# Optimization experiments

Measured on AMD Instinct MI355X. Metric: run time of the kernel, lower is better.

The kernel has to match this reference:

```python
import jax, jax.numpy as jnp
import numpy as np

N, K, D = 16384, 32, 256
NEG_SLOPE = 0.01  # torch F.leaky_relu default


def setup_inputs() -> dict:
    key = jax.random.key(0)
    k1, k2, k3, k4 = jax.random.split(key, 4)
    scale = 1.0 / np.sqrt(D)
    return {
        "target": jax.random.normal(k1, (N, D), dtype=jnp.float32),
        "middle": jax.random.normal(k2, (N, K, D), dtype=jnp.float32),
        "W": jax.random.normal(k3, (D, D), dtype=jnp.float32) * scale,
        "b": jnp.zeros((D,), dtype=jnp.float32),
        "a_w": jax.random.normal(k4, (1, D), dtype=jnp.float32) * scale,
        "a_b": jnp.zeros((1,), dtype=jnp.float32),
    }


def reference(target, middle, W, b, a_w, a_b):
    # attention_weight applied to both target and middle (bias added to each,
    # matching the torch code which sums two Linear outputs)
    pt = target @ W.T + b              # [N, D]
    pm = middle @ W.T + b              # [N, K, D]
    h = pt[:, None, :] + pm            # [N, K, D]
    # a_weight: D -> 1
    score = h @ a_w.T + a_b            # [N, K, 1]
    score = jax.nn.leaky_relu(score, negative_slope=NEG_SLOPE)
    coef = jax.nn.softmax(score, axis=-2)   # softmax over neighbor dim K
    neighbor_feature = jnp.sum(coef * middle, axis=-2)  # [N, D]
    return neighbor_feature
```

## Files before the change

kernel.cpp:

```cpp
#include <hip/hip_runtime.h>

#define N_ 16384
#define K_ 32
#define D_ 256
#define NEG_SLOPE 0.01f

__global__ __launch_bounds__(1024) void prep_kernel(
    const float* __restrict__ W, const float* __restrict__ b,
    const float* __restrict__ a_w, const float* __restrict__ a_b,
    float* __restrict__ ws) {
  __shared__ float part[4][D_];
  const int t = threadIdx.x;
  const int dd = t >> 8;
  const int e = t & 255;
  float acc = 0.f;
#pragma unroll 8
  for (int j = 0; j < 64; ++j) {
    const int d = dd * 64 + j;
    acc += a_w[d] * W[d * D_ + e];
  }
  part[dd][e] = acc;
  __syncthreads();
  if (t < D_) ws[t] = part[0][t] + part[1][t] + part[2][t] + part[3][t];
  __syncthreads();
  if (t < D_) part[0][t] = b[t] * a_w[t];
  __syncthreads();
  if (t == 0) {
    float s = 0.f;
    for (int i = 0; i < D_; ++i) s += part[0][i];
    ws[D_] = 2.f * s + a_b[0];
  }
}

__global__ __launch_bounds__(256) void attn_agg_kernel(
    const float* __restrict__ target, const float* __restrict__ middle,
    const float* __restrict__ ws, float* __restrict__ out) {
  __shared__ __align__(16) float smid[K_ * D_];
  __shared__ __align__(16) float lv[D_];
  __shared__ float sdot[K_];
  __shared__ float stp[4];
  __shared__ float scoef[K_];

  const int n = blockIdx.x;
  const int t = threadIdx.x;
  const int r = t >> 3;
  const int c = t & 7;

  lv[t] = ws[t];
  __syncthreads();

  const float4* mrow = (const float4*)(middle + (size_t)n * K_ * D_);
  float pdot = 0.f;
#pragma unroll
  for (int i = 0; i < 8; ++i) {
    const int s = c + i * 8;
    const float4 m4 = mrow[r * 64 + s];
    const float4 v4 = *(const float4*)(lv + s * 4);
    pdot += m4.x * v4.x + m4.y * v4.y + m4.z * v4.z + m4.w * v4.w;
    const int p = s ^ (r & 7);
    *(float4*)(smid + r * D_ + p * 4) = m4;
  }
  pdot += __shfl_xor(pdot, 1);
  pdot += __shfl_xor(pdot, 2);
  pdot += __shfl_xor(pdot, 4);
  if (c == 0) sdot[r] = pdot;

  float tp = target[(size_t)n * D_ + t] * lv[t];
#pragma unroll
  for (int off = 1; off < 64; off <<= 1) tp += __shfl_xor(tp, off);
  if ((t & 63) == 0) stp[t >> 6] = tp;
  __syncthreads();

  if (t < 64) {
    const float tdot = stp[0] + stp[1] + stp[2] + stp[3];
    const float cadd = ws[D_];
    const int k = t & 31;
    float sc = sdot[k] + tdot + cadd;
    sc = sc > 0.f ? sc : NEG_SLOPE * sc;
    float mx = sc;
    mx = fmaxf(mx, __shfl_xor(mx, 1));
    mx = fmaxf(mx, __shfl_xor(mx, 2));
    mx = fmaxf(mx, __shfl_xor(mx, 4));
    mx = fmaxf(mx, __shfl_xor(mx, 8));
    mx = fmaxf(mx, __shfl_xor(mx, 16));
    float ex = __expf(sc - mx);
    float sum = ex;
    sum += __shfl_xor(sum, 1);
    sum += __shfl_xor(sum, 2);
    sum += __shfl_xor(sum, 4);
    sum += __shfl_xor(sum, 8);
    sum += __shfl_xor(sum, 16);
    if (t < 32) scoef[k] = ex / sum;
  }
  __syncthreads();

  float acc = 0.f;
  const int s2 = t >> 2;
  const int e2 = t & 3;
#pragma unroll
  for (int k = 0; k < K_; ++k) {
    const int p = s2 ^ (k & 7);
    acc += scoef[k] * smid[k * D_ + p * 4 + e2];
  }
  out[(size_t)n * D_ + t] = acc;
}

extern "C" void kernel_launch(void* const* d_in, const int* in_sizes, int n_in,
                              void* d_out, int out_size, void* d_ws, size_t ws_size,
                              hipStream_t stream) {
  const float* target = (const float*)d_in[0];
  const float* middle = (const float*)d_in[1];
  const float* W      = (const float*)d_in[2];
  const float* b      = (const float*)d_in[3];
  const float* a_w    = (const float*)d_in[4];
  const float* a_b    = (const float*)d_in[5];
  float* out = (float*)d_out;
  float* ws  = (float*)d_ws;

  prep_kernel<<<1, 1024, 0, stream>>>(W, b, a_w, a_b, ws);
  attn_agg_kernel<<<N_, 256, 0, stream>>>(target, middle, ws, out);
}
```

Measured before the change: 111.1 us.

## Process eight rows per block with register double-buffered prefetch of next row

Each block now handles eight consecutive rows instead of one, with the grid reduced accordingly. While one row is processed through shared memory, the next row's middle and target data are already being loaded into registers (A/B ping-pong), overlapping global loads with compute. This aims to hide memory latency and amortize the per-block setup of loading the folded weight vector. The cost is higher register use (two 8-float4 buffers per thread), which may reduce occupancy, plus an extra barrier per row.

```diff
diff --git a/kernel.cpp b/kernel.cpp
--- a/kernel.cpp
+++ b/kernel.cpp
@@ -4,6 +4,9 @@
 #define K_ 32
 #define D_ 256
 #define NEG_SLOPE 0.01f
+
+#define GRID_ 2048
+#define ITER_ 8
 
 __global__ __launch_bounds__(1024) void prep_kernel(
     const float* __restrict__ W, const float* __restrict__ b,
@@ -32,40 +35,39 @@
   }
 }
 
-__global__ __launch_bounds__(256) void attn_agg_kernel(
-    const float* __restrict__ target, const float* __restrict__ middle,
-    const float* __restrict__ ws, float* __restrict__ out) {
-  __shared__ __align__(16) float smid[K_ * D_];
-  __shared__ __align__(16) float lv[D_];
-  __shared__ float sdot[K_];
-  __shared__ float stp[4];
-  __shared__ float scoef[K_];
+struct Buf {
+  float4 m[8];
+  float tg;
+};
 
-  const int n = blockIdx.x;
-  const int t = threadIdx.x;
-  const int r = t >> 3;
-  const int c = t & 7;
+__device__ __forceinline__ void load_buf(
+    Buf& bf, const float* __restrict__ middle, const float* __restrict__ target,
+    int n, int t, int r, int c) {
+  const float4* mrow = (const float4*)(middle + (size_t)n * K_ * D_);
+#pragma unroll
+  for (int i = 0; i < 8; ++i) bf.m[i] = mrow[r * 64 + c + i * 8];
+  bf.tg = target[(size_t)n * D_ + t];
+}
 
-  lv[t] = ws[t];
-  __syncthreads();
-
-  const float4* mrow = (const float4*)(middle + (size_t)n * K_ * D_);
+__device__ __forceinline__ void process(
+    const Buf& bf, float* __restrict__ smid, const float* __restrict__ lv,
+    float* __restrict__ sdot, float* __restrict__ stp, float* __restrict__ scoef,
+    float cadd, float* __restrict__ outrow, int t, int r, int c) {
   float pdot = 0.f;
 #pragma unroll
   for (int i = 0; i < 8; ++i) {
     const int s = c + i * 8;
-    const float4 m4 = mrow[r * 64 + s];
+    const float4 m4 = bf.m[i];
+    *(float4*)(smid + r * D_ + ((s ^ (r & 7)) * 4)) = m4;
     const float4 v4 = *(const float4*)(lv + s * 4);
     pdot += m4.x * v4.x + m4.y * v4.y + m4.z * v4.z + m4.w * v4.w;
-    const int p = s ^ (r & 7);
-    *(float4*)(smid + r * D_ + p * 4) = m4;
   }
   pdot += __shfl_xor(pdot, 1);
   pdot += __shfl_xor(pdot, 2);
   pdot += __shfl_xor(pdot, 4);
   if (c == 0) sdot[r] = pdot;
 
-  float tp = target[(size_t)n * D_ + t] * lv[t];
+  float tp = bf.tg * lv[t];
 #pragma unroll
   for (int off = 1; off < 64; off <<= 1) tp += __shfl_xor(tp, off);
   if ((t & 63) == 0) stp[t >> 6] = tp;
@@ -73,7 +75,6 @@
 
   if (t < 64) {
     const float tdot = stp[0] + stp[1] + stp[2] + stp[3];
-    const float cadd = ws[D_];
     const int k = t & 31;
     float sc = sdot[k] + tdot + cadd;
     sc = sc > 0.f ? sc : NEG_SLOPE * sc;
@@ -99,10 +100,44 @@
   const int e2 = t & 3;
 #pragma unroll
   for (int k = 0; k < K_; ++k) {
-    const int p = s2 ^ (k & 7);
-    acc += scoef[k] * smid[k * D_ + p * 4 + e2];
+    acc += scoef[k] * smid[k * D_ + ((s2 ^ (k & 7)) * 4) + e2];
   }
-  out[(size_t)n * D_ + t] = acc;
+  outrow[t] = acc;
+  __syncthreads();
+}
+
+__global__ __launch_bounds__(256) void attn_agg_kernel(
+    const float* __restrict__ target, const float* __restrict__ middle,
+    const float* __restrict__ ws, float* __restrict__ out) {
+  __shared__ __align__(16) float smid[K_ * D_];
+  __shared__ __align__(16) float lv[D_];
+  __shared__ float sdot[K_];
+  __shared__ float stp[4];
+  __shared__ float scoef[K_];
+
+  const int t = threadIdx.x;
+  const int r = t >> 3;
+  const int c = t & 7;
+
+  lv[t] = ws[t];
+  const float cadd = ws[D_];
+  __syncthreads();
+
+  const int n0 = blockIdx.x * ITER_;
+
+  Buf A, B;
+  load_buf(A, middle, target, n0, t, r, c);
+
+#pragma unroll 1
+  for (int it = 0; it < ITER_; it += 2) {
+    load_buf(B, middle, target, n0 + it + 1, t, r, c);
+    process(A, smid, lv, sdot, stp, scoef, cadd,
+            out + (size_t)(n0 + it) * D_, t, r, c);
+    if (it + 2 < ITER_)
+      load_buf(A, middle, target, n0 + it + 2, t, r, c);
+    process(B, smid, lv, sdot, stp, scoef, cadd,
+            out + (size_t)(n0 + it + 1) * D_, t, r, c);
+  }
 }
 
 extern "C" void kernel_launch(void* const* d_in, const int* in_sizes, int n_in,
@@ -118,5 +153,5 @@
   float* ws  = (float*)d_ws;
 
   prep_kernel<<<1, 1024, 0, stream>>>(W, b, a_w, a_b, ws);
-  attn_agg_kernel<<<N_, 256, 0, stream>>>(target, middle, ws, out);
+  attn_agg_kernel<<<GRID_, 256, 0, stream>>>(target, middle, ws, out);
 }
```

After: 123.5 us. 11.2% more time.

## Keep middle rows in registers instead of staging through shared memory

Applied to the files above, without the earlier changes.

Each warp now loads 8 neighbor rows of middle as float4 values into registers and computes the score dots with a transposed shuffle-reduction tree. The weighted sum is then done from registers, and the four partial sums per warp are combined through a small shared array. This removes the 32 KB shared-memory staging buffer and its swizzled reads and writes, which should raise occupancy and cut LDS traffic. The cost is higher register pressure from 32 live floats per thread, plus an extra barrier for the final reduction.

```diff
diff --git a/kernel.cpp b/kernel.cpp
--- a/kernel.cpp
+++ b/kernel.cpp
@@ -35,45 +35,62 @@
 __global__ __launch_bounds__(256) void attn_agg_kernel(
     const float* __restrict__ target, const float* __restrict__ middle,
     const float* __restrict__ ws, float* __restrict__ out) {
-  __shared__ __align__(16) float smid[K_ * D_];
-  __shared__ __align__(16) float lv[D_];
+  __shared__ __align__(16) float part[4][D_];
   __shared__ float sdot[K_];
+  __shared__ float scoef[K_];
   __shared__ float stp[4];
-  __shared__ float scoef[K_];
 
+  const int t = threadIdx.x;
+  const int kg = t >> 6;
+  const int l = t & 63;
   const int n = blockIdx.x;
-  const int t = threadIdx.x;
-  const int r = t >> 3;
-  const int c = t & 7;
 
-  lv[t] = ws[t];
-  __syncthreads();
+  const float4* m4p = (const float4*)(middle + (size_t)n * K_ * D_);
+  float4 m[8];
+#pragma unroll
+  for (int j = 0; j < 8; ++j) m[j] = m4p[(kg * 8 + j) * 64 + l];
 
-  const float4* mrow = (const float4*)(middle + (size_t)n * K_ * D_);
-  float pdot = 0.f;
+  const float4 vv = ((const float4*)ws)[l];
+  const float vt = ws[t];
+  const float cadd = ws[D_];
+  const float tg = target[(size_t)n * D_ + t];
+
+  float pd[8];
 #pragma unroll
-  for (int i = 0; i < 8; ++i) {
-    const int s = c + i * 8;
-    const float4 m4 = mrow[r * 64 + s];
-    const float4 v4 = *(const float4*)(lv + s * 4);
-    pdot += m4.x * v4.x + m4.y * v4.y + m4.z * v4.z + m4.w * v4.w;
-    const int p = s ^ (r & 7);
-    *(float4*)(smid + r * D_ + p * 4) = m4;
+  for (int j = 0; j < 8; ++j)
+    pd[j] = m[j].x * vv.x + m[j].y * vv.y + m[j].z * vv.z + m[j].w * vv.w;
+
+#pragma unroll
+  for (int j = 0; j < 8; ++j) pd[j] += __shfl_xor(pd[j], 32);
+  float q0 = (l & 32) ? pd[4] : pd[0];
+  float q1 = (l & 32) ? pd[5] : pd[1];
+  float q2 = (l & 32) ? pd[6] : pd[2];
+  float q3 = (l & 32) ? pd[7] : pd[3];
+  q0 += __shfl_xor(q0, 16);
+  q1 += __shfl_xor(q1, 16);
+  q2 += __shfl_xor(q2, 16);
+  q3 += __shfl_xor(q3, 16);
+  float r0 = (l & 16) ? q2 : q0;
+  float r1 = (l & 16) ? q3 : q1;
+  r0 += __shfl_xor(r0, 8);
+  r1 += __shfl_xor(r1, 8);
+  float s = (l & 8) ? r1 : r0;
+  s += __shfl_xor(s, 4);
+  s += __shfl_xor(s, 2);
+  s += __shfl_xor(s, 1);
+  if ((l & 7) == 0) {
+    const int j_own = ((l >> 5) & 1) * 4 + ((l >> 4) & 1) * 2 + ((l >> 3) & 1);
+    sdot[kg * 8 + j_own] = s;
   }
-  pdot += __shfl_xor(pdot, 1);
-  pdot += __shfl_xor(pdot, 2);
-  pdot += __shfl_xor(pdot, 4);
-  if (c == 0) sdot[r] = pdot;
 
-  float tp = target[(size_t)n * D_ + t] * lv[t];
+  float tp = tg * vt;
 #pragma unroll
   for (int off = 1; off < 64; off <<= 1) tp += __shfl_xor(tp, off);
-  if ((t & 63) == 0) stp[t >> 6] = tp;
+  if (l == 0) stp[kg] = tp;
   __syncthreads();
 
   if (t < 64) {
     const float tdot = stp[0] + stp[1] + stp[2] + stp[3];
-    const float cadd = ws[D_];
     const int k = t & 31;
     float sc = sdot[k] + tdot + cadd;
     sc = sc > 0.f ? sc : NEG_SLOPE * sc;
@@ -94,15 +111,19 @@
   }
   __syncthreads();
 
-  float acc = 0.f;
-  const int s2 = t >> 2;
-  const int e2 = t & 3;
+  float4 acc = make_float4(0.f, 0.f, 0.f, 0.f);
 #pragma unroll
-  for (int k = 0; k < K_; ++k) {
-    const int p = s2 ^ (k & 7);
-    acc += scoef[k] * smid[k * D_ + p * 4 + e2];
+  for (int j = 0; j < 8; ++j) {
+    const float cf = scoef[kg * 8 + j];
+    acc.x += cf * m[j].x;
+    acc.y += cf * m[j].y;
+    acc.z += cf * m[j].z;
+    acc.w += cf * m[j].w;
   }
-  out[(size_t)n * D_ + t] = acc;
+  *(float4*)(&part[kg][4 * l]) = acc;
+  __syncthreads();
+
+  out[(size_t)n * D_ + t] = part[0][t] + part[1][t] + part[2][t] + part[3][t];
 }
 
 extern "C" void kernel_launch(void* const* d_in, const int* in_sizes, int n_in,
```

Result: slower. 113.7 us (+2.3%).
